# Kernel optimization log

Measured on AMD Instinct MI355X. Metric: run time of the kernel, lower is better.

Reference implementation:

```python
import jax, jax.numpy as jnp
import numpy as np

D = 1024
H = 16
HD = D // H
MLP = 4 * D


def _lin(key, fin, fout):
    k1, k2 = jax.random.split(key)
    lim = 1.0 / np.sqrt(fin)
    W = jax.random.uniform(k1, (fin, fout), minval=-lim, maxval=lim, dtype=jnp.float32)
    b = jax.random.uniform(k2, (fout,), minval=-lim, maxval=lim, dtype=jnp.float32)
    return W, b


def setup_inputs() -> dict:
    key = jax.random.key(0)
    ks = jax.random.split(key, 10)
    x = jax.random.normal(ks[0], (4, 2048, D), dtype=jnp.float32)
    time_emb = jax.random.normal(ks[1], (4, D), dtype=jnp.float32)
    Wqkv, bqkv = _lin(ks[2], D, 3 * D)
    Wproj, bproj = _lin(ks[3], D, D)
    W1, b1 = _lin(ks[4], D, MLP)
    W2, b2 = _lin(ks[5], MLP, D)
    Wt, bt = _lin(ks[6], D, 6 * D)
    g1 = jnp.ones((D,), jnp.float32); be1 = jnp.zeros((D,), jnp.float32)
    g2 = jnp.ones((D,), jnp.float32); be2 = jnp.zeros((D,), jnp.float32)
    return {"x": x, "time_emb": time_emb, "Wqkv": Wqkv, "bqkv": bqkv,
            "Wproj": Wproj, "bproj": bproj, "W1": W1, "b1": b1, "W2": W2, "b2": b2,
            "Wt": Wt, "bt": bt, "g1": g1, "be1": be1, "g2": g2, "be2": be2}


def layernorm(x, g, b, eps=1e-5):
    mu = jnp.mean(x, axis=-1, keepdims=True)
    var = jnp.var(x, axis=-1, keepdims=True)
    return (x - mu) * jax.lax.rsqrt(var + eps) * g + b


def attention(h, Wqkv, bqkv, Wproj, bproj):
    B, L, _ = h.shape
    qkv = (h @ Wqkv + bqkv).reshape(B, L, 3, H, HD)
    q, k, v = jnp.moveaxis(qkv, 2, 0)  # each [B,L,H,HD]
    scale = HD ** -0.5
    attn = jnp.einsum('blhd,bmhd->bhlm', q, k) * scale
    attn = jax.nn.softmax(attn, axis=-1)
    out = jnp.einsum('bhlm,bmhd->blhd', attn, v).reshape(B, L, D)
    return out @ Wproj + bproj


def reference(x, time_emb, Wqkv, bqkv, Wproj, bproj, W1, b1, W2, b2, Wt, bt, g1, be1, g2, be2):
    tp = (jax.nn.silu(time_emb) @ Wt + bt)[:, None, :]  # [B,1,6D]
    shift_msa, scale_msa, gate_msa, shift_mlp, scale_mlp, gate_mlp = jnp.split(tp, 6, axis=-1)
    h = layernorm(x, g1, be1)
    h = h * (1.0 + scale_msa) + shift_msa
    h = attention(h, Wqkv, bqkv, Wproj, bproj)
    x = x + gate_msa * h
    h = layernorm(x, g2, be2)
    h = h * (1.0 + scale_mlp) + shift_mlp
    h = jax.nn.gelu(h @ W1 + b1, approximate=False) @ W2 + b2
    x = x + gate_mlp * h
    return x
```

## Files before the change

kernel.cpp:

```cpp
#include <hip/hip_runtime.h>
#include <hip/hip_bf16.h>
#include <math.h>


typedef __attribute__((ext_vector_type(8))) __bf16 bf16x8;
typedef __attribute__((ext_vector_type(4))) float f32x4;

union FragU { uint4 u; bf16x8 b; };

#define AS1(p) ((const __attribute__((address_space(1))) void*)(p))
#define AS3(p) ((__attribute__((address_space(3))) void*)(p))

__device__ __forceinline__ float bflo(uint u) {
    union { uint i; float f; } v; v.i = u << 16; return v.f;
}
__device__ __forceinline__ ushort f2bf(float f) {
    union { float f; uint i; } v; v.f = f;
    uint r = (v.i + 0x7fffu + ((v.i >> 16) & 1u)) >> 16;
    return (ushort)r;
}
__device__ __forceinline__ uint pkbf(float a, float b) {
    return __builtin_amdgcn_perm(__float_as_uint(b), __float_as_uint(a), 0x07060302u);
}
__device__ __forceinline__ void stval(ushort* p, float v) { *p = f2bf(v); }
__device__ __forceinline__ void stval(float* p, float v) { *p = v; }

__device__ __forceinline__ float gelu_f(float x) {
    float y = 0.7978845608f * (x + 0.044715f * x * x * x);
    float e = exp2f(y * 2.88539008178f);
    float t = 1.f - 2.f / (1.f + e);
    return 0.5f * x * (1.f + t);
}

__global__ __launch_bounds__(256) void transpose_f2b(const float* __restrict__ in,
                                                     ushort* __restrict__ out,
                                                     int R, int C) {
    __shared__ ushort t[32][33];
    int c0 = blockIdx.x * 32, r0 = blockIdx.y * 32;
    int tx = threadIdx.x, ty = threadIdx.y;
#pragma unroll
    for (int i = 0; i < 32; i += 8)
        t[ty + i][tx] = f2bf(in[(size_t)(r0 + ty + i) * C + c0 + tx]);
    __syncthreads();
#pragma unroll
    for (int i = 0; i < 32; i += 8)
        out[(size_t)(c0 + ty + i) * R + r0 + tx] = t[tx][ty + i];
}

__global__ __launch_bounds__(256) void transpose_v(const ushort* __restrict__ qkv,
                                                   ushort* __restrict__ vT) {
    int bh = blockIdx.x >> 5, lt = blockIdx.x & 31;
    int b = bh >> 4, h = bh & 15;
    int d = threadIdx.x & 63, lg = threadIdx.x >> 6;
    const ushort* src = qkv + (size_t)b * 2048 * 3072 + 2048 + h * 64 + d;
#pragma unroll
    for (int g = 0; g < 2; g++) {
        int l0 = lt * 64 + lg * 16 + g * 8;
        ushort v[8];
#pragma unroll
        for (int i = 0; i < 8; i++) v[i] = src[(size_t)(l0 + i) * 3072];
        *(uint4*)&vT[((size_t)bh * 64 + d) * 2048 + l0] = *(uint4*)v;
    }
}

__global__ __launch_bounds__(256) void tp_gemm(const float* __restrict__ te,
                                               const ushort* __restrict__ WtT,
                                               const float* __restrict__ bt,
                                               float* __restrict__ tp) {
    int w = blockIdx.x * 4 + (threadIdx.x >> 6);
    int lane = threadIdx.x & 63;
    int b = w / 6144, n = w % 6144;
    const ushort* wr = WtT + (size_t)n * 1024;
    const float* tr = te + (size_t)b * 1024;
    float s = 0.f;
#pragma unroll
    for (int i = 0; i < 16; i++) {
        int k = lane + 64 * i;
        float t = tr[k];
        float sil = t / (1.f + __expf(-t));
        s += sil * bflo((uint)wr[k]);
    }
#pragma unroll
    for (int x = 32; x; x >>= 1) s += __shfl_xor(s, x);
    if (lane == 0) tp[(size_t)b * 6144 + n] = s + bt[n];
}

__global__ __launch_bounds__(256) void ln_mod(const float* __restrict__ x,
                                              const float* __restrict__ tpb,
                                              const float* __restrict__ g,
                                              const float* __restrict__ be,
                                              ushort* __restrict__ out,
                                              int shift_off, int scale_off) {
    __shared__ float2 sred[4];
    int row = blockIdx.x;
    int b = row >> 11;
    int tid = threadIdx.x;
    float4 f = *(const float4*)&x[(size_t)row * 1024 + tid * 4];
    float v[4] = {f.x, f.y, f.z, f.w};
    float s = v[0] + v[1] + v[2] + v[3];
    float s2 = v[0] * v[0] + v[1] * v[1] + v[2] * v[2] + v[3] * v[3];
#pragma unroll
    for (int m = 32; m; m >>= 1) { s += __shfl_xor(s, m); s2 += __shfl_xor(s2, m); }
    if ((tid & 63) == 0) sred[tid >> 6] = make_float2(s, s2);
    __syncthreads();
    s = sred[0].x + sred[1].x + sred[2].x + sred[3].x;
    s2 = sred[0].y + sred[1].y + sred[2].y + sred[3].y;
    float mu = s * (1.f / 1024.f);
    float var = s2 * (1.f / 1024.f) - mu * mu;
    float rs = rsqrtf(var + 1e-5f);
    const float* tprow = tpb + (size_t)b * 6144;
    ushort o4[4];
#pragma unroll
    for (int t = 0; t < 4; t++) {
        int c = tid * 4 + t;
        float y = (v[t] - mu) * rs * g[c] + be[c];
        y = y * (1.f + tprow[scale_off + c]) + tprow[shift_off + c];
        o4[t] = f2bf(y);
    }
    *(uint2*)&out[(size_t)row * 1024 + tid * 4] = *(uint2*)o4;
}

template <int EPI, typename OT>
__global__ __launch_bounds__(256) void gemm_bt(const ushort* __restrict__ A,
                                               const ushort* __restrict__ BT,
                                               const float* __restrict__ bias,
                                               OT* __restrict__ C,
                                               int M, int N, int K,
                                               const float* __restrict__ res,
                                               const float* __restrict__ tpb,
                                               int goff, int sccols) {
    __shared__ __align__(16) ushort As[2][128 * 32];
    __shared__ __align__(16) ushort Bs[2][128 * 32];
    int m0 = blockIdx.y * 128, n0 = blockIdx.x * 128;
    int tid = threadIdx.x;
    int wid = tid >> 6, lane = tid & 63;
    int wy = wid >> 1, wx = wid & 1;
    int r16 = lane & 15;
    int q8 = (lane >> 4) << 3;

    f32x4 acc[4][4];
#pragma unroll
    for (int i = 0; i < 4; i++)
#pragma unroll
        for (int j = 0; j < 4; j++) acc[i][j] = (f32x4){0.f, 0.f, 0.f, 0.f};

    int sr = tid >> 2;
    int sc = (tid & 3) << 3;
    const ushort* Abase = A + (size_t)(m0 + sr) * K + sc;
    const ushort* Bbase = BT + (size_t)(n0 + sr) * K + sc;

    for (int k0 = 0; k0 < K; k0 += 64) {
#pragma unroll
        for (int c = 0; c < 2; c++) {
            ushort* AsW = As[c] + wid * 512;
            ushort* BsW = Bs[c] + wid * 512;
            int kk = k0 + 32 * c;
            __builtin_amdgcn_global_load_lds(AS1(Abase + kk), AS3(AsW), 16, 0, 0);
            __builtin_amdgcn_global_load_lds(AS1(Abase + (size_t)64 * K + kk), AS3(AsW + 2048), 16, 0, 0);
            __builtin_amdgcn_global_load_lds(AS1(Bbase + kk), AS3(BsW), 16, 0, 0);
            __builtin_amdgcn_global_load_lds(AS1(Bbase + (size_t)64 * K + kk), AS3(BsW + 2048), 16, 0, 0);
        }
        __syncthreads();
#pragma unroll
        for (int c = 0; c < 2; c++) {
            FragU fa[4], fb[4];
#pragma unroll
            for (int i = 0; i < 4; i++)
                fa[i].u = *(const uint4*)&As[c][(wy * 64 + i * 16 + r16) * 32 + q8];
#pragma unroll
            for (int j = 0; j < 4; j++)
                fb[j].u = *(const uint4*)&Bs[c][(wx * 64 + j * 16 + r16) * 32 + q8];
#pragma unroll
            for (int i = 0; i < 4; i++)
#pragma unroll
                for (int j = 0; j < 4; j++)
                    acc[i][j] = __builtin_amdgcn_mfma_f32_16x16x32_bf16(fa[i].b, fb[j].b, acc[i][j], 0, 0, 0);
        }
        __syncthreads();
    }

    int q4 = (lane >> 4) << 2;
#pragma unroll
    for (int i = 0; i < 4; i++) {
#pragma unroll
        for (int j = 0; j < 4; j++) {
            int col = n0 + wx * 64 + j * 16 + r16;
            float bv = bias[col];
#pragma unroll
            for (int t = 0; t < 4; t++) {
                int row = m0 + wy * 64 + i * 16 + q4 + t;
                float v = acc[i][j][t] + bv;
                if constexpr (EPI == 0) {
                    if (col < sccols) v *= 0.18033688011f;
                }
                if constexpr (EPI == 1) {
                    v = gelu_f(v);
                }
                if constexpr (EPI == 2) {
                    float rv = res[(size_t)row * N + col];
                    float gate = tpb[(size_t)(row >> 11) * 6144 + goff + col];
                    v = rv + gate * v;
                }
                stval(&C[(size_t)row * N + col], v);
            }
        }
    }
}

template <int EPI>
__global__ __launch_bounds__(512, 2) void gemm_8ph(const ushort* __restrict__ A,
                                                   const ushort* __restrict__ BT,
                                                   const float* __restrict__ bias,
                                                   ushort* __restrict__ C,
                                                   int M, int N, int K, int sccols) {
    __shared__ __align__(16) ushort La[2][256 * 64];
    __shared__ __align__(16) ushort Lb[2][256 * 64];
    int tid = threadIdx.x;
    int wid = tid >> 6, lane = tid & 63;
    int wm = wid >> 2, wn = wid & 3;
    int r16 = lane & 15;
    int q8 = (lane >> 4) << 3, q4 = (lane >> 4) << 2;
    int m0 = blockIdx.y * 256, n0 = blockIdx.x * 256;

    int sr = tid >> 3;
    int sc = (tid & 7) << 3;
    int scs = sc ^ ((sr & 7) << 3);
    const ushort* Ab = A + (size_t)(m0 + sr) * K + scs;
    const ushort* Bb = BT + (size_t)(n0 + sr) * K + scs;

    int sxor = (r16 & 7) << 3;

    f32x4 acc[8][4];
#pragma unroll
    for (int i = 0; i < 8; i++)
#pragma unroll
        for (int j = 0; j < 4; j++) acc[i][j] = (f32x4){0.f, 0.f, 0.f, 0.f};

    auto STAGE = [&](int t) {
        int p = t & 1;
        int kk = t << 6;
#pragma unroll
        for (int i = 0; i < 4; i++) {
            __builtin_amdgcn_global_load_lds(AS1(Ab + (size_t)i * 64 * K + kk),
                                             AS3(&La[p][i * 4096 + wid * 512]), 16, 0, 0);
            __builtin_amdgcn_global_load_lds(AS1(Bb + (size_t)i * 64 * K + kk),
                                             AS3(&Lb[p][i * 4096 + wid * 512]), 16, 0, 0);
        }
    };

    int NT = K >> 6;
    STAGE(0);
    STAGE(1);
    asm volatile("s_waitcnt vmcnt(8)" ::: "memory");
    __builtin_amdgcn_sched_barrier(0);
    __builtin_amdgcn_s_barrier();

    for (int t = 0; t < NT; t++) {
        int cur = t & 1;
        const ushort* la = La[cur];
        const ushort* lb = Lb[cur];
        FragU fa[4][2], fb[4][2], fa2[4][2];
#pragma unroll
        for (int i = 0; i < 4; i++)
#pragma unroll
            for (int kk = 0; kk < 2; kk++)
                fa[i][kk].u = *(const uint4*)&la[(wm * 128 + i * 16 + r16) * 64 + ((kk * 32 + q8) ^ sxor)];
#pragma unroll
        for (int j = 0; j < 4; j++)
#pragma unroll
            for (int kk = 0; kk < 2; kk++)
                fb[j][kk].u = *(const uint4*)&lb[(wn * 64 + j * 16 + r16) * 64 + ((kk * 32 + q8) ^ sxor)];
        __builtin_amdgcn_s_setprio(1);
#pragma unroll
        for (int i = 0; i < 4; i++)
#pragma unroll
            for (int j = 0; j < 4; j++)
#pragma unroll
                for (int kk = 0; kk < 2; kk++)
                    acc[i][j] = __builtin_amdgcn_mfma_f32_16x16x32_bf16(fa[i][kk].b, fb[j][kk].b, acc[i][j], 0, 0, 0);
        __builtin_amdgcn_s_setprio(0);
#pragma unroll
        for (int i = 0; i < 4; i++)
#pragma unroll
            for (int kk = 0; kk < 2; kk++)
                fa2[i][kk].u = *(const uint4*)&la[(wm * 128 + 64 + i * 16 + r16) * 64 + ((kk * 32 + q8) ^ sxor)];
        __builtin_amdgcn_s_setprio(1);
#pragma unroll
        for (int i = 0; i < 4; i++)
#pragma unroll
            for (int j = 0; j < 2; j++)
#pragma unroll
                for (int kk = 0; kk < 2; kk++)
                    acc[4 + i][j] = __builtin_amdgcn_mfma_f32_16x16x32_bf16(fa2[i][kk].b, fb[j][kk].b, acc[4 + i][j], 0, 0, 0);
        __builtin_amdgcn_s_setprio(0);
        asm volatile("s_waitcnt lgkmcnt(0)" ::: "memory");
        __builtin_amdgcn_sched_barrier(0);
        __builtin_amdgcn_s_barrier();
        if (t + 2 < NT) STAGE(t + 2);
        __builtin_amdgcn_s_setprio(1);
#pragma unroll
        for (int i = 0; i < 4; i++)
#pragma unroll
            for (int j = 2; j < 4; j++)
#pragma unroll
                for (int kk = 0; kk < 2; kk++)
                    acc[4 + i][j] = __builtin_amdgcn_mfma_f32_16x16x32_bf16(fa2[i][kk].b, fb[j][kk].b, acc[4 + i][j], 0, 0, 0);
        __builtin_amdgcn_s_setprio(0);
        if (t + 2 < NT) {
            asm volatile("s_waitcnt vmcnt(8)" ::: "memory");
        } else {
            asm volatile("s_waitcnt vmcnt(0)" ::: "memory");
        }
        __builtin_amdgcn_sched_barrier(0);
        __builtin_amdgcn_s_barrier();
    }

#pragma unroll
    for (int i = 0; i < 8; i++) {
        int rbase = m0 + wm * 128 + (i >> 2) * 64 + (i & 3) * 16 + q4;
#pragma unroll
        for (int j = 0; j < 4; j++) {
            int col = n0 + wn * 64 + j * 16 + r16;
            float bv = bias[col];
#pragma unroll
            for (int tt = 0; tt < 4; tt++) {
                float v = acc[i][j][tt] + bv;
                if constexpr (EPI == 0) {
                    if (col < sccols) v *= 0.18033688011f;
                }
                if constexpr (EPI == 1) {
                    v = gelu_f(v);
                }
                C[(size_t)(rbase + tt) * N + col] = f2bf(v);
            }
        }
    }
}

__global__ __launch_bounds__(512, 4) void attn_mfma(const ushort* __restrict__ qkv,
                                                    const ushort* __restrict__ vT,
                                                    ushort* __restrict__ out) {
    __shared__ __align__(16) ushort Ks[2][64 * 72];
    __shared__ __align__(16) ushort Vs[2][64 * 72];
    __shared__ __align__(16) ushort Ps[256 * 72];

    int tid = threadIdx.x;
    int wid = tid >> 6, lane = tid & 63;
    int r16 = lane & 15, quad = lane >> 4;
    int q8 = quad << 3, q4 = quad << 2;

    int bh = blockIdx.x >> 3;
    int qt = blockIdx.x & 7;
    int b = bh >> 4, h = bh & 15;
    const ushort* qkbase = qkv + (size_t)b * 2048 * 3072 + h * 64;

    int kr = tid >> 3;
    int kc = (tid & 7) << 3;
    const ushort* kptr = qkbase + 1024 + (size_t)kr * 3072 + kc;
    const ushort* vptr = vT + (size_t)bh * 131072 + (size_t)kr * 2048 + kc;

    uint4 ka = *(const uint4*)kptr;
    uint4 va = *(const uint4*)vptr;

    {
        int r = tid >> 1;
        int c = (tid & 1) << 5;
        const ushort* qp = qkbase + (size_t)(qt * 256 + r) * 3072 + c;
        *(uint4*)&Ps[r * 72 + c]      = *(const uint4*)qp;
        *(uint4*)&Ps[r * 72 + c + 8]  = *(const uint4*)(qp + 8);
        *(uint4*)&Ps[r * 72 + c + 16] = *(const uint4*)(qp + 16);
        *(uint4*)&Ps[r * 72 + c + 24] = *(const uint4*)(qp + 24);
    }
    __syncthreads();
    FragU qa[2][2];
#pragma unroll
    for (int qm = 0; qm < 2; qm++)
#pragma unroll
        for (int ks = 0; ks < 2; ks++)
            qa[qm][ks].u = *(const uint4*)&Ps[(wid * 32 + qm * 16 + r16) * 72 + ks * 32 + q8];

    *(uint4*)&Ks[0][kr * 72 + kc] = ka;
    *(uint4*)&Vs[0][kr * 72 + kc] = va;
    ka = *(const uint4*)(kptr + (size_t)64 * 3072);
    va = *(const uint4*)(vptr + 64);
    __syncthreads();

    float l4[2][4] = {{0.f, 0.f, 0.f, 0.f}, {0.f, 0.f, 0.f, 0.f}};
    f32x4 o[2][4];
#pragma unroll
    for (int qm = 0; qm < 2; qm++)
#pragma unroll
        for (int dn = 0; dn < 4; dn++) o[qm][dn] = (f32x4){0.f, 0.f, 0.f, 0.f};

    for (int kt = 0; kt < 32; kt++) {
        int cur = kt & 1;
        const ushort* ksb = Ks[cur];
        const ushort* vsb = Vs[cur];

        if (kt < 31) {
            *(uint4*)&Ks[cur ^ 1][kr * 72 + kc] = ka;
            *(uint4*)&Vs[cur ^ 1][kr * 72 + kc] = va;
        }

        FragU kb[2][4];
#pragma unroll
        for (int ks = 0; ks < 2; ks++)
#pragma unroll
            for (int n = 0; n < 4; n++)
                kb[ks][n].u = *(const uint4*)&ksb[(n * 16 + r16) * 72 + ks * 32 + q8];
#pragma unroll
        for (int qm = 0; qm < 2; qm++) {
            f32x4 s[4];
#pragma unroll
            for (int n = 0; n < 4; n++) s[n] = (f32x4){0.f, 0.f, 0.f, 0.f};
#pragma unroll
            for (int ks = 0; ks < 2; ks++)
#pragma unroll
                for (int n = 0; n < 4; n++)
                    s[n] = __builtin_amdgcn_mfma_f32_16x16x32_bf16(kb[ks][n].b, qa[qm][ks].b, s[n], 0, 0, 0);
#pragma unroll
            for (int n = 0; n < 4; n++) {
                float p0 = exp2f(s[n][0]);
                float p1 = exp2f(s[n][1]);
                float p2 = exp2f(s[n][2]);
                float p3 = exp2f(s[n][3]);
                l4[qm][0] += p0; l4[qm][1] += p1; l4[qm][2] += p2; l4[qm][3] += p3;
                uint2 w2 = make_uint2(pkbf(p0, p1), pkbf(p2, p3));
                *(uint2*)&Ps[(wid * 32 + qm * 16 + r16) * 72 + n * 16 + q4] = w2;
            }
        }

        if (kt < 30) {
            ka = *(const uint4*)(kptr + (size_t)(kt + 2) * 64 * 3072);
            va = *(const uint4*)(vptr + (kt + 2) * 64);
        }

#pragma unroll
        for (int ks = 0; ks < 2; ks++) {
            FragU vb[4], pa0, pa1;
#pragma unroll
            for (int dn = 0; dn < 4; dn++)
                vb[dn].u = *(const uint4*)&vsb[(dn * 16 + r16) * 72 + ks * 32 + q8];
            pa0.u = *(const uint4*)&Ps[(wid * 32 + r16) * 72 + ks * 32 + q8];
            pa1.u = *(const uint4*)&Ps[(wid * 32 + 16 + r16) * 72 + ks * 32 + q8];
#pragma unroll
            for (int dn = 0; dn < 4; dn++) {
                o[0][dn] = __builtin_amdgcn_mfma_f32_16x16x32_bf16(vb[dn].b, pa0.b, o[0][dn], 0, 0, 0);
                o[1][dn] = __builtin_amdgcn_mfma_f32_16x16x32_bf16(vb[dn].b, pa1.b, o[1][dn], 0, 0, 0);
            }
        }

        __syncthreads();
    }

#pragma unroll
    for (int qm = 0; qm < 2; qm++) {
        float l_ = (l4[qm][0] + l4[qm][1]) + (l4[qm][2] + l4[qm][3]);
        l_ += __shfl_xor(l_, 16);
        l_ += __shfl_xor(l_, 32);
        float inv = 1.f / l_;
        int row = qt * 256 + wid * 32 + qm * 16 + r16;
        ushort* orow = out + (size_t)(b * 2048 + row) * 1024 + h * 64;
#pragma unroll
        for (int dn = 0; dn < 4; dn++) {
            uint2 w2 = make_uint2(pkbf(o[qm][dn][0] * inv, o[qm][dn][1] * inv),
                                  pkbf(o[qm][dn][2] * inv, o[qm][dn][3] * inv));
            *(uint2*)&orow[dn * 16 + q4] = w2;
        }
    }
}

extern "C" void kernel_launch(void* const* d_in, const int* in_sizes, int n_in,
                              void* d_out, int out_size, void* d_ws, size_t ws_size,
                              hipStream_t stream) {
    const float* x    = (const float*)d_in[0];
    const float* te   = (const float*)d_in[1];
    const float* Wqkv = (const float*)d_in[2];
    const float* bqkv = (const float*)d_in[3];
    const float* Wproj= (const float*)d_in[4];
    const float* bproj= (const float*)d_in[5];
    const float* W1   = (const float*)d_in[6];
    const float* b1   = (const float*)d_in[7];
    const float* W2   = (const float*)d_in[8];
    const float* b2   = (const float*)d_in[9];
    const float* Wt   = (const float*)d_in[10];
    const float* bt   = (const float*)d_in[11];
    const float* g1   = (const float*)d_in[12];
    const float* be1  = (const float*)d_in[13];
    const float* g2   = (const float*)d_in[14];
    const float* be2  = (const float*)d_in[15];

    char* ws = (char*)d_ws;
    ushort* WqkvT  = (ushort*)(ws + 0);
    ushort* WprojT = (ushort*)(ws + 6291456);
    ushort* W1T    = (ushort*)(ws + 8388608);
    ushort* W2T    = (ushort*)(ws + 16777216);
    ushort* WtT    = (ushort*)(ws + 25165824);
    float*  tpb    = (float*)(ws + 37748736);
    ushort* hbuf   = (ushort*)(ws + 37847040);
    ushort* vTb    = (ushort*)(ws + 37847040);
    ushort* qkvb   = (ushort*)(ws + 54624256);
    ushort* midb   = (ushort*)(ws + 54624256);
    ushort* attnb  = (ushort*)(ws + 121733120);
    float*  x1b    = (float*)(ws + 138510336);

    dim3 tb(32, 8);
    hipLaunchKernelGGL(transpose_f2b, dim3(3072 / 32, 1024 / 32), tb, 0, stream, Wqkv, WqkvT, 1024, 3072);
    hipLaunchKernelGGL(transpose_f2b, dim3(1024 / 32, 1024 / 32), tb, 0, stream, Wproj, WprojT, 1024, 1024);
    hipLaunchKernelGGL(transpose_f2b, dim3(4096 / 32, 1024 / 32), tb, 0, stream, W1, W1T, 1024, 4096);
    hipLaunchKernelGGL(transpose_f2b, dim3(1024 / 32, 4096 / 32), tb, 0, stream, W2, W2T, 4096, 1024);
    hipLaunchKernelGGL(transpose_f2b, dim3(6144 / 32, 1024 / 32), tb, 0, stream, Wt, WtT, 1024, 6144);

    hipLaunchKernelGGL(tp_gemm, dim3(6144), dim3(256), 0, stream, te, WtT, bt, tpb);

    hipLaunchKernelGGL(ln_mod, dim3(8192), dim3(256), 0, stream, x, tpb, g1, be1, hbuf, 0, 1024);

    hipLaunchKernelGGL((gemm_8ph<0>), dim3(3072 / 256, 8192 / 256), dim3(512), 0, stream,
                       hbuf, WqkvT, bqkv, qkvb, 8192, 3072, 1024, 1024);

    hipLaunchKernelGGL(transpose_v, dim3(2048), dim3(256), 0, stream, qkvb, vTb);

    hipLaunchKernelGGL(attn_mfma, dim3(512), dim3(512), 0, stream, qkvb, vTb, attnb);

    hipLaunchKernelGGL((gemm_bt<2, float>), dim3(1024 / 128, 8192 / 128), dim3(256), 0, stream,
                       attnb, WprojT, bproj, x1b, 8192, 1024, 1024, x, tpb, 2048, 0);

    hipLaunchKernelGGL(ln_mod, dim3(8192), dim3(256), 0, stream, x1b, tpb, g2, be2, hbuf, 3072, 4096);

    hipLaunchKernelGGL((gemm_8ph<1>), dim3(4096 / 256, 8192 / 256), dim3(512), 0, stream,
                       hbuf, W1T, b1, midb, 8192, 4096, 1024, 0);

    hipLaunchKernelGGL((gemm_bt<2, float>), dim3(1024 / 128, 8192 / 128), dim3(256), 0, stream,
                       midb, W2T, b2, (float*)d_out, 8192, 1024, 4096, x1b, tpb, 5120, 0);
}
```

Before: 588.9 us.

## Route projection and MLP-down GEMMs through pipelined 8-wave kernel; MFMA row sums

Generalizes the 8-wave double-buffered, swizzled-LDS GEMM to a templated N tile (256 or 128) with residual/gate epilogue. The projection and W2 GEMMs now use it with 256x128 tiles, replacing the simple 128x128 kernel that synchronized twice per step. The aim is better MFMA utilization and overlap of global loads with compute. Separately, attention drops the scalar exp accumulation and shuffles and gets the softmax denominator from an extra MFMA against a ones vector. That adds MFMA work, and the sum now uses the bf16-rounded probabilities.

```diff
diff --git a/kernel.cpp b/kernel.cpp
--- a/kernel.cpp
+++ b/kernel.cpp
@@ -120,76 +120,165 @@
     *(uint2*)&out[(size_t)row * 1024 + tid * 4] = *(uint2*)o4;
 }
 
-template <int EPI, typename OT>
-__global__ __launch_bounds__(256) void gemm_bt(const ushort* __restrict__ A,
-                                               const ushort* __restrict__ BT,
-                                               const float* __restrict__ bias,
-                                               OT* __restrict__ C,
-                                               int M, int N, int K,
-                                               const float* __restrict__ res,
-                                               const float* __restrict__ tpb,
-                                               int goff, int sccols) {
-    __shared__ __align__(16) ushort As[2][128 * 32];
-    __shared__ __align__(16) ushort Bs[2][128 * 32];
-    int m0 = blockIdx.y * 128, n0 = blockIdx.x * 128;
+template <int EPI, int BN, typename OT>
+__global__ __launch_bounds__(512, 2) void gemm_8ph(const ushort* __restrict__ A,
+                                                   const ushort* __restrict__ BT,
+                                                   const float* __restrict__ bias,
+                                                   OT* __restrict__ C,
+                                                   int M, int N, int K,
+                                                   const float* __restrict__ res,
+                                                   const float* __restrict__ tpb,
+                                                   int goff, int sccols) {
+    constexpr int WN = BN / 64;
+    constexpr int WM = 8 / WN;
+    constexpr int RW = 256 / WM;
+    constexpr int G  = RW / 64;
+    constexpr int BLOADS = (BN * 64 * 2) / (512 * 16);
+    constexpr int SLOADS = 4 + BLOADS;
+
+    __shared__ __align__(16) ushort La[2][256 * 64];
+    __shared__ __align__(16) ushort Lb[2][BN * 64];
     int tid = threadIdx.x;
     int wid = tid >> 6, lane = tid & 63;
-    int wy = wid >> 1, wx = wid & 1;
+    int wm = wid / WN, wn = wid % WN;
     int r16 = lane & 15;
-    int q8 = (lane >> 4) << 3;
-
-    f32x4 acc[4][4];
-#pragma unroll
-    for (int i = 0; i < 4; i++)
+    int q8 = (lane >> 4) << 3, q4 = (lane >> 4) << 2;
+    int m0 = blockIdx.y * 256, n0 = blockIdx.x * BN;
+
+    int sr = tid >> 3;
+    int sc = (tid & 7) << 3;
+    int scs = sc ^ ((sr & 7) << 3);
+    const ushort* Ab = A + (size_t)(m0 + sr) * K + scs;
+    const ushort* Bb = BT + (size_t)(n0 + sr) * K + scs;
+
+    int sxor = (r16 & 7) << 3;
+
+    f32x4 acc[4 * G][4];
+#pragma unroll
+    for (int i = 0; i < 4 * G; i++)
 #pragma unroll
         for (int j = 0; j < 4; j++) acc[i][j] = (f32x4){0.f, 0.f, 0.f, 0.f};
 
-    int sr = tid >> 2;
-    int sc = (tid & 3) << 3;
-    const ushort* Abase = A + (size_t)(m0 + sr) * K + sc;
-    const ushort* Bbase = BT + (size_t)(n0 + sr) * K + sc;
-
-    for (int k0 = 0; k0 < K; k0 += 64) {
-#pragma unroll
-        for (int c = 0; c < 2; c++) {
-            ushort* AsW = As[c] + wid * 512;
-            ushort* BsW = Bs[c] + wid * 512;
-            int kk = k0 + 32 * c;
-            __builtin_amdgcn_global_load_lds(AS1(Abase + kk), AS3(AsW), 16, 0, 0);
-            __builtin_amdgcn_global_load_lds(AS1(Abase + (size_t)64 * K + kk), AS3(AsW + 2048), 16, 0, 0);
-            __builtin_amdgcn_global_load_lds(AS1(Bbase + kk), AS3(BsW), 16, 0, 0);
-            __builtin_amdgcn_global_load_lds(AS1(Bbase + (size_t)64 * K + kk), AS3(BsW + 2048), 16, 0, 0);
-        }
-        __syncthreads();
-#pragma unroll
-        for (int c = 0; c < 2; c++) {
-            FragU fa[4], fb[4];
-#pragma unroll
-            for (int i = 0; i < 4; i++)
-                fa[i].u = *(const uint4*)&As[c][(wy * 64 + i * 16 + r16) * 32 + q8];
-#pragma unroll
-            for (int j = 0; j < 4; j++)
-                fb[j].u = *(const uint4*)&Bs[c][(wx * 64 + j * 16 + r16) * 32 + q8];
+    auto STAGE = [&](int t) {
+        int p = t & 1;
+        int kk = t << 6;
+#pragma unroll
+        for (int i = 0; i < 4; i++)
+            __builtin_amdgcn_global_load_lds(AS1(Ab + (size_t)i * 64 * K + kk),
+                                             AS3(&La[p][i * 4096 + wid * 512]), 16, 0, 0);
+#pragma unroll
+        for (int i = 0; i < BLOADS; i++)
+            __builtin_amdgcn_global_load_lds(AS1(Bb + (size_t)i * 64 * K + kk),
+                                             AS3(&Lb[p][i * 4096 + wid * 512]), 16, 0, 0);
+    };
+
+    int NT = K >> 6;
+    STAGE(0);
+    STAGE(1);
+    if constexpr (SLOADS == 8) asm volatile("s_waitcnt vmcnt(8)" ::: "memory");
+    else                       asm volatile("s_waitcnt vmcnt(6)" ::: "memory");
+    __builtin_amdgcn_sched_barrier(0);
+    __builtin_amdgcn_s_barrier();
+
+    for (int t = 0; t < NT; t++) {
+        int cur = t & 1;
+        const ushort* la = La[cur];
+        const ushort* lb = Lb[cur];
+        FragU fa[4][2], fb[4][2];
+#pragma unroll
+        for (int i = 0; i < 4; i++)
+#pragma unroll
+            for (int kk = 0; kk < 2; kk++)
+                fa[i][kk].u = *(const uint4*)&la[(wm * RW + i * 16 + r16) * 64 + ((kk * 32 + q8) ^ sxor)];
+#pragma unroll
+        for (int j = 0; j < 4; j++)
+#pragma unroll
+            for (int kk = 0; kk < 2; kk++)
+                fb[j][kk].u = *(const uint4*)&lb[(wn * 64 + j * 16 + r16) * 64 + ((kk * 32 + q8) ^ sxor)];
+
+        if constexpr (G == 2) {
+            FragU fa2[4][2];
+            __builtin_amdgcn_s_setprio(1);
 #pragma unroll
             for (int i = 0; i < 4; i++)
 #pragma unroll
                 for (int j = 0; j < 4; j++)
-                    acc[i][j] = __builtin_amdgcn_mfma_f32_16x16x32_bf16(fa[i].b, fb[j].b, acc[i][j], 0, 0, 0);
-        }
-        __syncthreads();
-    }
-
-    int q4 = (lane >> 4) << 2;
-#pragma unroll
-    for (int i = 0; i < 4; i++) {
+#pragma unroll
+                    for (int kk = 0; kk < 2; kk++)
+                        acc[i][j] = __builtin_amdgcn_mfma_f32_16x16x32_bf16(fa[i][kk].b, fb[j][kk].b, acc[i][j], 0, 0, 0);
+            __builtin_amdgcn_s_setprio(0);
+#pragma unroll
+            for (int i = 0; i < 4; i++)
+#pragma unroll
+                for (int kk = 0; kk < 2; kk++)
+                    fa2[i][kk].u = *(const uint4*)&la[(wm * RW + 64 + i * 16 + r16) * 64 + ((kk * 32 + q8) ^ sxor)];
+            __builtin_amdgcn_s_setprio(1);
+#pragma unroll
+            for (int i = 0; i < 4; i++)
+#pragma unroll
+                for (int j = 0; j < 2; j++)
+#pragma unroll
+                    for (int kk = 0; kk < 2; kk++)
+                        acc[4 + i][j] = __builtin_amdgcn_mfma_f32_16x16x32_bf16(fa2[i][kk].b, fb[j][kk].b, acc[4 + i][j], 0, 0, 0);
+            __builtin_amdgcn_s_setprio(0);
+            asm volatile("s_waitcnt lgkmcnt(0)" ::: "memory");
+            __builtin_amdgcn_sched_barrier(0);
+            __builtin_amdgcn_s_barrier();
+            if (t + 2 < NT) STAGE(t + 2);
+            __builtin_amdgcn_s_setprio(1);
+#pragma unroll
+            for (int i = 0; i < 4; i++)
+#pragma unroll
+                for (int j = 2; j < 4; j++)
+#pragma unroll
+                    for (int kk = 0; kk < 2; kk++)
+                        acc[4 + i][j] = __builtin_amdgcn_mfma_f32_16x16x32_bf16(fa2[i][kk].b, fb[j][kk].b, acc[4 + i][j], 0, 0, 0);
+            __builtin_amdgcn_s_setprio(0);
+        } else {
+            __builtin_amdgcn_s_setprio(1);
+#pragma unroll
+            for (int i = 0; i < 4; i++)
+#pragma unroll
+                for (int j = 0; j < 2; j++)
+#pragma unroll
+                    for (int kk = 0; kk < 2; kk++)
+                        acc[i][j] = __builtin_amdgcn_mfma_f32_16x16x32_bf16(fa[i][kk].b, fb[j][kk].b, acc[i][j], 0, 0, 0);
+            __builtin_amdgcn_s_setprio(0);
+            asm volatile("s_waitcnt lgkmcnt(0)" ::: "memory");
+            __builtin_amdgcn_sched_barrier(0);
+            __builtin_amdgcn_s_barrier();
+            if (t + 2 < NT) STAGE(t + 2);
+            __builtin_amdgcn_s_setprio(1);
+#pragma unroll
+            for (int i = 0; i < 4; i++)
+#pragma unroll
+                for (int j = 2; j < 4; j++)
+#pragma unroll
+                    for (int kk = 0; kk < 2; kk++)
+                        acc[i][j] = __builtin_amdgcn_mfma_f32_16x16x32_bf16(fa[i][kk].b, fb[j][kk].b, acc[i][j], 0, 0, 0);
+            __builtin_amdgcn_s_setprio(0);
+        }
+        if (t + 2 < NT) {
+            if constexpr (SLOADS == 8) asm volatile("s_waitcnt vmcnt(8)" ::: "memory");
+            else                       asm volatile("s_waitcnt vmcnt(6)" ::: "memory");
+        } else {
+            asm volatile("s_waitcnt vmcnt(0)" ::: "memory");
+        }
+        __builtin_amdgcn_sched_barrier(0);
+        __builtin_amdgcn_s_barrier();
+    }
+
+#pragma unroll
+    for (int i = 0; i < 4 * G; i++) {
+        int rbase = m0 + wm * RW + (i >> 2) * 64 + (i & 3) * 16 + q4;
 #pragma unroll
         for (int j = 0; j < 4; j++) {
-            int col = n0 + wx * 64 + j * 16 + r16;
+            int col = n0 + wn * 64 + j * 16 + r16;
             float bv = bias[col];
 #pragma unroll
-            for (int t = 0; t < 4; t++) {
-                int row = m0 + wy * 64 + i * 16 + q4 + t;
-                float v = acc[i][j][t] + bv;
+            for (int tt = 0; tt < 4; tt++) {
+                int row = rbase + tt;
+                float v = acc[i][j][tt] + bv;
                 if constexpr (EPI == 0) {
                     if (col < sccols) v *= 0.18033688011f;
                 }
@@ -207,136 +296,6 @@
     }
 }
 
-template <int EPI>
-__global__ __launch_bounds__(512, 2) void gemm_8ph(const ushort* __restrict__ A,
-                                                   const ushort* __restrict__ BT,
-                                                   const float* __restrict__ bias,
-                                                   ushort* __restrict__ C,
-                                                   int M, int N, int K, int sccols) {
-    __shared__ __align__(16) ushort La[2][256 * 64];
-    __shared__ __align__(16) ushort Lb[2][256 * 64];
-    int tid = threadIdx.x;
-    int wid = tid >> 6, lane = tid & 63;
-    int wm = wid >> 2, wn = wid & 3;
-    int r16 = lane & 15;
-    int q8 = (lane >> 4) << 3, q4 = (lane >> 4) << 2;
-    int m0 = blockIdx.y * 256, n0 = blockIdx.x * 256;
-
-    int sr = tid >> 3;
-    int sc = (tid & 7) << 3;
-    int scs = sc ^ ((sr & 7) << 3);
-    const ushort* Ab = A + (size_t)(m0 + sr) * K + scs;
-    const ushort* Bb = BT + (size_t)(n0 + sr) * K + scs;
-
-    int sxor = (r16 & 7) << 3;
-
-    f32x4 acc[8][4];
-#pragma unroll
-    for (int i = 0; i < 8; i++)
-#pragma unroll
-        for (int j = 0; j < 4; j++) acc[i][j] = (f32x4){0.f, 0.f, 0.f, 0.f};
-
-    auto STAGE = [&](int t) {
-        int p = t & 1;
-        int kk = t << 6;
-#pragma unroll
-        for (int i = 0; i < 4; i++) {
-            __builtin_amdgcn_global_load_lds(AS1(Ab + (size_t)i * 64 * K + kk),
-                                             AS3(&La[p][i * 4096 + wid * 512]), 16, 0, 0);
-            __builtin_amdgcn_global_load_lds(AS1(Bb + (size_t)i * 64 * K + kk),
-                                             AS3(&Lb[p][i * 4096 + wid * 512]), 16, 0, 0);
-        }
-    };
-
-    int NT = K >> 6;
-    STAGE(0);
-    STAGE(1);
-    asm volatile("s_waitcnt vmcnt(8)" ::: "memory");
-    __builtin_amdgcn_sched_barrier(0);
-    __builtin_amdgcn_s_barrier();
-
-    for (int t = 0; t < NT; t++) {
-        int cur = t & 1;
-        const ushort* la = La[cur];
-        const ushort* lb = Lb[cur];
-        FragU fa[4][2], fb[4][2], fa2[4][2];
-#pragma unroll
-        for (int i = 0; i < 4; i++)
-#pragma unroll
-            for (int kk = 0; kk < 2; kk++)
-                fa[i][kk].u = *(const uint4*)&la[(wm * 128 + i * 16 + r16) * 64 + ((kk * 32 + q8) ^ sxor)];
-#pragma unroll
-        for (int j = 0; j < 4; j++)
-#pragma unroll
-            for (int kk = 0; kk < 2; kk++)
-                fb[j][kk].u = *(const uint4*)&lb[(wn * 64 + j * 16 + r16) * 64 + ((kk * 32 + q8) ^ sxor)];
-        __builtin_amdgcn_s_setprio(1);
-#pragma unroll
-        for (int i = 0; i < 4; i++)
-#pragma unroll
-            for (int j = 0; j < 4; j++)
-#pragma unroll
-                for (int kk = 0; kk < 2; kk++)
-                    acc[i][j] = __builtin_amdgcn_mfma_f32_16x16x32_bf16(fa[i][kk].b, fb[j][kk].b, acc[i][j], 0, 0, 0);
-        __builtin_amdgcn_s_setprio(0);
-#pragma unroll
-        for (int i = 0; i < 4; i++)
-#pragma unroll
-            for (int kk = 0; kk < 2; kk++)
-                fa2[i][kk].u = *(const uint4*)&la[(wm * 128 + 64 + i * 16 + r16) * 64 + ((kk * 32 + q8) ^ sxor)];
-        __builtin_amdgcn_s_setprio(1);
-#pragma unroll
-        for (int i = 0; i < 4; i++)
-#pragma unroll
-            for (int j = 0; j < 2; j++)
-#pragma unroll
-                for (int kk = 0; kk < 2; kk++)
-                    acc[4 + i][j] = __builtin_amdgcn_mfma_f32_16x16x32_bf16(fa2[i][kk].b, fb[j][kk].b, acc[4 + i][j], 0, 0, 0);
-        __builtin_amdgcn_s_setprio(0);
-        asm volatile("s_waitcnt lgkmcnt(0)" ::: "memory");
-        __builtin_amdgcn_sched_barrier(0);
-        __builtin_amdgcn_s_barrier();
-        if (t + 2 < NT) STAGE(t + 2);
-        __builtin_amdgcn_s_setprio(1);
-#pragma unroll
-        for (int i = 0; i < 4; i++)
-#pragma unroll
-            for (int j = 2; j < 4; j++)
-#pragma unroll
-                for (int kk = 0; kk < 2; kk++)
-                    acc[4 + i][j] = __builtin_amdgcn_mfma_f32_16x16x32_bf16(fa2[i][kk].b, fb[j][kk].b, acc[4 + i][j], 0, 0, 0);
-        __builtin_amdgcn_s_setprio(0);
-        if (t + 2 < NT) {
-            asm volatile("s_waitcnt vmcnt(8)" ::: "memory");
-        } else {
-            asm volatile("s_waitcnt vmcnt(0)" ::: "memory");
-        }
-        __builtin_amdgcn_sched_barrier(0);
-        __builtin_amdgcn_s_barrier();
-    }
-
-#pragma unroll
-    for (int i = 0; i < 8; i++) {
-        int rbase = m0 + wm * 128 + (i >> 2) * 64 + (i & 3) * 16 + q4;
-#pragma unroll
-        for (int j = 0; j < 4; j++) {
-            int col = n0 + wn * 64 + j * 16 + r16;
-            float bv = bias[col];
-#pragma unroll
-            for (int tt = 0; tt < 4; tt++) {
-                float v = acc[i][j][tt] + bv;
-                if constexpr (EPI == 0) {
-                    if (col < sccols) v *= 0.18033688011f;
-                }
-                if constexpr (EPI == 1) {
-                    v = gelu_f(v);
-                }
-                C[(size_t)(rbase + tt) * N + col] = f2bf(v);
-            }
-        }
-    }
-}
-
 __global__ __launch_bounds__(512, 4) void attn_mfma(const ushort* __restrict__ qkv,
                                                     const ushort* __restrict__ vT,
                                                     ushort* __restrict__ out) {
@@ -385,7 +344,9 @@
     va = *(const uint4*)(vptr + 64);
     __syncthreads();
 
-    float l4[2][4] = {{0.f, 0.f, 0.f, 0.f}, {0.f, 0.f, 0.f, 0.f}};
+    FragU onesf;
+    onesf.u = make_uint4(0x3F803F80u, 0x3F803F80u, 0x3F803F80u, 0x3F803F80u);
+    f32x4 lacc[2] = {(f32x4){0.f, 0.f, 0.f, 0.f}, (f32x4){0.f, 0.f, 0.f, 0.f}};
     f32x4 o[2][4];
 #pragma unroll
     for (int qm = 0; qm < 2; qm++)
@@ -420,12 +381,8 @@
                     s[n] = __builtin_amdgcn_mfma_f32_16x16x32_bf16(kb[ks][n].b, qa[qm][ks].b, s[n], 0, 0, 0);
 #pragma unroll
             for (int n = 0; n < 4; n++) {
-                float p0 = exp2f(s[n][0]);
-                float p1 = exp2f(s[n][1]);
-                float p2 = exp2f(s[n][2]);
-                float p3 = exp2f(s[n][3]);
-                l4[qm][0] += p0; l4[qm][1] += p1; l4[qm][2] += p2; l4[qm][3] += p3;
-                uint2 w2 = make_uint2(pkbf(p0, p1), pkbf(p2, p3));
+                uint2 w2 = make_uint2(pkbf(exp2f(s[n][0]), exp2f(s[n][1])),
+                                      pkbf(exp2f(s[n][2]), exp2f(s[n][3])));
                 *(uint2*)&Ps[(wid * 32 + qm * 16 + r16) * 72 + n * 16 + q4] = w2;
             }
         }
@@ -448,6 +405,8 @@
                 o[0][dn] = __builtin_amdgcn_mfma_f32_16x16x32_bf16(vb[dn].b, pa0.b, o[0][dn], 0, 0, 0);
                 o[1][dn] = __builtin_amdgcn_mfma_f32_16x16x32_bf16(vb[dn].b, pa1.b, o[1][dn], 0, 0, 0);
             }
+            lacc[0] = __builtin_amdgcn_mfma_f32_16x16x32_bf16(onesf.b, pa0.b, lacc[0], 0, 0, 0);
+            lacc[1] = __builtin_amdgcn_mfma_f32_16x16x32_bf16(onesf.b, pa1.b, lacc[1], 0, 0, 0);
         }
 
         __syncthreads();
@@ -455,10 +414,7 @@
 
 #pragma unroll
     for (int qm = 0; qm < 2; qm++) {
-        float l_ = (l4[qm][0] + l4[qm][1]) + (l4[qm][2] + l4[qm][3]);
-        l_ += __shfl_xor(l_, 16);
-        l_ += __shfl_xor(l_, 32);
-        float inv = 1.f / l_;
+        float inv = 1.f / lacc[qm][0];
         int row = qt * 256 + wid * 32 + qm * 16 + r16;
         ushort* orow = out + (size_t)(b * 2048 + row) * 1024 + h * 64;
 #pragma unroll
@@ -515,21 +471,23 @@
 
     hipLaunchKernelGGL(ln_mod, dim3(8192), dim3(256), 0, stream, x, tpb, g1, be1, hbuf, 0, 1024);
 
-    hipLaunchKernelGGL((gemm_8ph<0>), dim3(3072 / 256, 8192 / 256), dim3(512), 0, stream,
-                       hbuf, WqkvT, bqkv, qkvb, 8192, 3072, 1024, 1024);
+    hipLaunchKernelGGL((gemm_8ph<0, 256, ushort>), dim3(3072 / 256, 8192 / 256), dim3(512), 0, stream,
+                       hbuf, WqkvT, bqkv, qkvb, 8192, 3072, 1024,
+                       (const float*)nullptr, (const float*)nullptr, 0, 1024);
 
     hipLaunchKernelGGL(transpose_v, dim3(2048), dim3(256), 0, stream, qkvb, vTb);
 
     hipLaunchKernelGGL(attn_mfma, dim3(512), dim3(512), 0, stream, qkvb, vTb, attnb);
 
-    hipLaunchKernelGGL((gemm_bt<2, float>), dim3(1024 / 128, 8192 / 128), dim3(256), 0, stream,
+    hipLaunchKernelGGL((gemm_8ph<2, 128, float>), dim3(1024 / 128, 8192 / 256), dim3(512), 0, stream,
                        attnb, WprojT, bproj, x1b, 8192, 1024, 1024, x, tpb, 2048, 0);
 
     hipLaunchKernelGGL(ln_mod, dim3(8192), dim3(256), 0, stream, x1b, tpb, g2, be2, hbuf, 3072, 4096);
 
-    hipLaunchKernelGGL((gemm_8ph<1>), dim3(4096 / 256, 8192 / 256), dim3(512), 0, stream,
-                       hbuf, W1T, b1, midb, 8192, 4096, 1024, 0);
-
-    hipLaunchKernelGGL((gemm_bt<2, float>), dim3(1024 / 128, 8192 / 128), dim3(256), 0, stream,
+    hipLaunchKernelGGL((gemm_8ph<1, 256, ushort>), dim3(4096 / 256, 8192 / 256), dim3(512), 0, stream,
+                       hbuf, W1T, b1, midb, 8192, 4096, 1024,
+                       (const float*)nullptr, (const float*)nullptr, 0, 0);
+
+    hipLaunchKernelGGL((gemm_8ph<2, 128, float>), dim3(1024 / 128, 8192 / 256), dim3(512), 0, stream,
                        midb, W2T, b2, (float*)d_out, 8192, 1024, 4096, x1b, tpb, 5120, 0);
 }
```

Measured after the change: 588.4 us. No clear change (-0.1%).
